# Kernel tuning notes

Hardware: AMD Instinct MI355X
Metric: run time of the kernel (lower is better)

The kernel has to match this reference:

```python
import jax, jax.numpy as jnp
import numpy as np

B = 65536
HIDDEN = 1024
NUM_LABELS = 30
MAX_OUT = 19
LABEL_IDS = [
    [0, 1, 2, 3, 5, 7, 19, 20, 28],
    [0, 1, 2, 3, 5, 7, 19, 20, 28],
    [0, 5, 7, 18, 19, 20, 22],
    [0, 1, 2, 3, 5, 7, 19, 20],
    [0, 1, 2, 3, 5, 7, 19, 20, 28],
    [0, 1, 2, 3, 5, 7, 9, 20],
    [0, 2, 4, 6, 8, 10, 12, 13, 14, 15, 16, 17, 21, 24, 26, 27],
    [0, 4, 6, 8, 10, 11, 12, 13, 14, 15, 17, 23, 24, 26, 27, 29],
    [0, 4, 6, 10, 11, 14, 15, 17, 21, 24, 25, 26, 27],
    [0, 4, 6, 7, 8, 10, 11, 12, 13, 14, 15, 17, 21, 23, 24, 26, 27, 28, 29],
    [0, 4, 6, 8, 10, 11, 12, 13, 14, 15, 16, 17, 21, 27, 29],
    [0, 4, 6, 10, 12, 15, 21, 24, 25],
]
# static remap: for head i, label l -> candidates.index(l) if present else 0
_REMAP = np.zeros((12, NUM_LABELS), dtype=np.int32)
for _i, _cand in enumerate(LABEL_IDS):
    for _j, _c in enumerate(_cand):
        _REMAP[_i, _c] = _j
REMAP = jnp.asarray(_REMAP)


def setup_inputs() -> dict:
    key = jax.random.key(0)
    k1, k2, k3, k4, k5 = jax.random.split(key, 5)
    features = jax.random.normal(k1, (B, HIDDEN), dtype=jnp.float32)
    Ws = jax.random.normal(k2, (12, HIDDEN, MAX_OUT), dtype=jnp.float32) * 0.02
    bs = jax.random.normal(k3, (12, MAX_OUT), dtype=jnp.float32) * 0.02
    head_ids = jax.random.randint(k4, (B,), 0, 12, dtype=jnp.int32)
    labels = jax.random.randint(k5, (B,), 0, NUM_LABELS, dtype=jnp.int32)
    return {"features": features, "Ws": Ws, "bs": bs,
            "head_ids": head_ids, "labels": labels}


def reference(features, Ws, bs, head_ids, labels):
    bsz = features.shape[0]
    h = jnp.tanh(features)  # FCLayer: dropout(p=0) -> tanh -> linear
    scattered = []
    total_loss = jnp.float32(0.0)
    for i, cand in enumerate(LABEL_IDS):
        n = len(cand)
        logit = h @ Ws[i][:, :n] + bs[i][:n]  # [B, n] small GEMM
        # scatter head logits into full 30-label space (base fill 1e-7)
        idx = jnp.asarray(cand, dtype=jnp.int32)
        z = jnp.full((bsz, NUM_LABELS), 1e-7, dtype=logit.dtype).at[:, idx].set(logit)
        scattered.append(z)
        # weighted CE over remapped labels (weight 0.05 for class 0, 1 otherwise)
        y = REMAP[i][labels]  # [B]
        logp = jax.nn.log_softmax(logit, axis=-1)
        nll = -jnp.take_along_axis(logp, y[:, None], axis=1)[:, 0]
        w = jnp.where(y == 0, jnp.float32(0.05), jnp.float32(1.0))
        total_loss = total_loss + jnp.sum(w * nll) / jnp.sum(w)
    cat_logits = jnp.stack(scattered, axis=1)  # [B, 12, 30]
    logits = cat_logits[jnp.arange(bsz), head_ids]  # gather by head id -> [B, 30]
    return total_loss, logits
```

## Files before the change

### kernel.cpp

```cpp
#include <hip/hip_runtime.h>
#include <cstdint>

typedef __attribute__((ext_vector_type(8)))  __bf16 bf16x8;
typedef __attribute__((ext_vector_type(16))) float  f32x16;

namespace {

constexpr int NHEADS = 12;
constexpr int TOT    = 138;
constexpr int NLBL   = 30;
constexpr int HID    = 1024;
constexpr int MAXO   = 19;
constexpr int NPAD   = 160;
constexpr int KB     = 16;
constexpr int NT     = HID / KB;
constexpr int TILE_ELE = NPAD * KB;
constexpr int EPS    = 161;

constexpr int HOFF[NHEADS + 1] = {0, 9, 18, 25, 33, 42, 50, 66, 82, 95, 114, 129, 138};
constexpr int NI[NHEADS] = {9, 9, 7, 8, 9, 8, 16, 16, 13, 19, 15, 9};
constexpr int CAND[TOT] = {
    0, 1, 2, 3, 5, 7, 19, 20, 28,
    0, 1, 2, 3, 5, 7, 19, 20, 28,
    0, 5, 7, 18, 19, 20, 22,
    0, 1, 2, 3, 5, 7, 19, 20,
    0, 1, 2, 3, 5, 7, 19, 20, 28,
    0, 1, 2, 3, 5, 7, 9, 20,
    0, 2, 4, 6, 8, 10, 12, 13, 14, 15, 16, 17, 21, 24, 26, 27,
    0, 4, 6, 8, 10, 11, 12, 13, 14, 15, 17, 23, 24, 26, 27, 29,
    0, 4, 6, 10, 11, 14, 15, 17, 21, 24, 25, 26, 27,
    0, 4, 6, 7, 8, 10, 11, 12, 13, 14, 15, 17, 21, 23, 24, 26, 27, 28, 29,
    0, 4, 6, 8, 10, 11, 12, 13, 14, 15, 16, 17, 21, 27, 29,
    0, 4, 6, 10, 12, 15, 21, 24, 25};

__device__ __forceinline__ float fast_tanh(float x) {
    float e = __expf(2.0f * x);
    return 1.0f - 2.0f * __builtin_amdgcn_rcpf(e + 1.0f);
}

__device__ __forceinline__ void head_of(int c, int& i, int& base) {
    if      (c <   9) { i = 0;  base = 0;   }
    else if (c <  18) { i = 1;  base = 9;   }
    else if (c <  25) { i = 2;  base = 18;  }
    else if (c <  33) { i = 3;  base = 25;  }
    else if (c <  42) { i = 4;  base = 33;  }
    else if (c <  50) { i = 5;  base = 42;  }
    else if (c <  66) { i = 6;  base = 50;  }
    else if (c <  82) { i = 7;  base = 66;  }
    else if (c <  95) { i = 8;  base = 82;  }
    else if (c < 114) { i = 9;  base = 95;  }
    else if (c < 129) { i = 10; base = 114; }
    else              { i = 11; base = 129; }
}

}

__global__ void pack_w_split(const float* __restrict__ Ws,
                             __bf16* __restrict__ Wh, __bf16* __restrict__ Wl) {
    const int t = blockIdx.x;
    for (int e = threadIdx.x; e < TILE_ELE; e += 256) {
        const int c  = e >> 4;
        const int kk = e & 15;
        float w = 0.0f;
        if (c < TOT) {
            int i, base;
            head_of(c, i, base);
            w = Ws[((size_t)i * HID + t * KB + kk) * MAXO + (c - base)];
        }
        __bf16 hi = (__bf16)w;
        Wh[(size_t)t * TILE_ELE + e] = hi;
        Wl[(size_t)t * TILE_ELE + e] = (__bf16)(w - (float)hi);
    }
}

__global__ __launch_bounds__(128, 1)
void fused_mfma(const float* __restrict__ F,
                const __bf16* __restrict__ Wph,
                const __bf16* __restrict__ Wpl,
                const float* __restrict__ bs,
                const int* __restrict__ head_ids,
                const int* __restrict__ labels,
                float* __restrict__ out,
                double* __restrict__ partials)
{
    __shared__ __align__(16) __bf16 htH[128 * KB];
    __shared__ __align__(16) __bf16 htL[128 * KB];
    __shared__ __align__(16) float  ep[64 * EPS];
    __shared__ float zbuf[64 * NLBL];

    const int tid  = threadIdx.x;
    const int wv   = tid >> 6;
    const int lane = tid & 63;
    const int brow = blockIdx.x * 128;

    const float* __restrict__ frow = F + (size_t)(brow + tid) * HID;
    const int boff = (lane & 31) * KB + (lane >> 5) * 8;

    f32x16 acc[2][5];
#pragma unroll
    for (int mt = 0; mt < 2; ++mt)
#pragma unroll
        for (int n = 0; n < 5; ++n)
#pragma unroll
            for (int r = 0; r < 16; ++r) acc[mt][n][r] = 0.0f;

    float4 fbA[4], fbB[4];
    bf16x8 BhA[5], BlA[5], BhB[5], BlB[5];

    {
        const float4* fp = (const float4*)frow;
#pragma unroll
        for (int q = 0; q < 4; ++q) fbA[q] = fp[q];
#pragma unroll
        for (int n = 0; n < 5; ++n) {
            BhA[n] = *(const bf16x8*)(Wph + boff + n * 512);
            BlA[n] = *(const bf16x8*)(Wpl + boff + n * 512);
        }
    }

#define STEP(FC, BHC, BLC, FN, BHN, BLN, T)                                    \
    {                                                                          \
        if ((T) + 1 < NT) {                                                    \
            const float4* fp_ = (const float4*)(frow + ((T) + 1) * KB);        \
            _Pragma("unroll") for (int q = 0; q < 4; ++q) FN[q] = fp_[q];      \
            const size_t wo_ = (size_t)((T) + 1) * TILE_ELE + boff;            \
            _Pragma("unroll") for (int n = 0; n < 5; ++n) {                    \
                BHN[n] = *(const bf16x8*)(Wph + wo_ + n * 512);                \
                BLN[n] = *(const bf16x8*)(Wpl + wo_ + n * 512);                \
            }                                                                  \
        }                                                                      \
        __syncthreads();                \
        {                                                                      \
            bf16x8 vh0, vh1, vl0, vl1;                                         \
            _Pragma("unroll") for (int q = 0; q < 4; ++q) {                    \
                float vx[4] = {FC[q].x, FC[q].y, FC[q].z, FC[q].w};            \
                _Pragma("unroll") for (int e = 0; e < 4; ++e) {                \
                    const int j = q * 4 + e;                                   \
                    float hv = fast_tanh(vx[e]);                               \
                    __bf16 hh = (__bf16)hv;                                    \
                    __bf16 hl = (__bf16)(hv - (float)hh);                      \
                    if (j < 8) { vh0[j] = hh; vl0[j] = hl; }                   \
                    else       { vh1[j - 8] = hh; vl1[j - 8] = hl; }           \
                }                                                              \
            }                                                                  \
            *(bf16x8*)&htH[tid * KB]     = vh0;                                \
            *(bf16x8*)&htH[tid * KB + 8] = vh1;                                \
            *(bf16x8*)&htL[tid * KB]     = vl0;                                \
            *(bf16x8*)&htL[tid * KB + 8] = vl1;                                \
        }                                                                      \
        __syncthreads();                                     \
        _Pragma("unroll") for (int mt = 0; mt < 2; ++mt) {                     \
            const int ab_ = (wv * 64 + mt * 32 + (lane & 31)) * KB +           \
                            (lane >> 5) * 8;                                   \
            bf16x8 ah = *(const bf16x8*)&htH[ab_];                             \
            bf16x8 al = *(const bf16x8*)&htL[ab_];                             \
            _Pragma("unroll") for (int n = 0; n < 5; ++n) {                    \
                acc[mt][n] = __builtin_amdgcn_mfma_f32_32x32x16_bf16(          \
                    ah, BHC[n], acc[mt][n], 0, 0, 0);                          \
                acc[mt][n] = __builtin_amdgcn_mfma_f32_32x32x16_bf16(          \
                    al, BHC[n], acc[mt][n], 0, 0, 0);                          \
                acc[mt][n] = __builtin_amdgcn_mfma_f32_32x32x16_bf16(          \
                    ah, BLC[n], acc[mt][n], 0, 0, 0);                          \
            }                                                                  \
        }                                                                      \
    }

    for (int t = 0; t < NT; t += 2) {
        STEP(fbA, BhA, BlA, fbB, BhB, BlB, t);
        STEP(fbB, BhB, BlB, fbA, BhA, BlA, t + 1);
    }
#undef STEP

    float wnacc[NHEADS], wdacc[NHEADS];
#pragma unroll
    for (int i = 0; i < NHEADS; ++i) { wnacc[i] = 0.0f; wdacc[i] = 0.0f; }

#pragma unroll 1
    for (int pass = 0; pass < 2; ++pass) {
        __syncthreads();
        if (wv == pass) {
#pragma unroll
            for (int mt = 0; mt < 2; ++mt)
#pragma unroll
                for (int n = 0; n < 5; ++n)
#pragma unroll
                    for (int r = 0; r < 16; ++r) {
                        const int rl = mt * 32 + (r & 3) + 8 * (r >> 2) + 4 * (lane >> 5);
                        ep[rl * EPS + n * 32 + (lane & 31)] = acc[mt][n][r];
                    }
        }
        __syncthreads();

        if (tid < 64) {
            const int row = brow + pass * 64 + tid;
            float a[TOT];
#pragma unroll
            for (int c = 0; c < TOT; ++c) a[c] = ep[tid * EPS + c];

#pragma unroll
            for (int i = 0; i < NHEADS; ++i)
#pragma unroll
                for (int j = 0; j < MAXO; ++j)
                    if (j < NI[i]) a[HOFF[i] + j] += bs[i * MAXO + j];

            const int label = labels[row];
            const int head  = head_ids[row];

#pragma unroll
            for (int i = 0; i < NHEADS; ++i) {
                int y = 0;
#pragma unroll
                for (int j = 0; j < MAXO; ++j)
                    if (j < NI[i]) { if (CAND[HOFF[i] + j] == label) y = j; }

                float m = a[HOFF[i]];
#pragma unroll
                for (int j = 1; j < MAXO; ++j)
                    if (j < NI[i]) m = fmaxf(m, a[HOFF[i] + j]);
                float s = 0.0f;
#pragma unroll
                for (int j = 0; j < MAXO; ++j)
                    if (j < NI[i]) s += __expf(a[HOFF[i] + j] - m);
                float lse = m + __logf(s);

                float ly = a[HOFF[i]];
#pragma unroll
                for (int j = 1; j < MAXO; ++j)
                    if (j < NI[i]) ly = (y == j) ? a[HOFF[i] + j] : ly;

                float w = (y == 0) ? 0.05f : 1.0f;
                wnacc[i] += w * (lse - ly);
                wdacc[i] += w;
            }

            float v[NLBL];
#pragma unroll
            for (int l = 0; l < NLBL; ++l) v[l] = 1e-7f;
#pragma unroll
            for (int i = 0; i < NHEADS; ++i) {
                if (head == i) {
#pragma unroll
                    for (int j = 0; j < MAXO; ++j)
                        if (j < NI[i]) v[CAND[HOFF[i] + j]] = a[HOFF[i] + j];
                }
            }
#pragma unroll
            for (int l = 0; l < NLBL; ++l) zbuf[tid * NLBL + l] = v[l];
        }
        __syncthreads();

        float* __restrict__ dst = out + 1 + (size_t)(brow + pass * 64) * NLBL;
        for (int q = tid; q < 64 * NLBL; q += 128) dst[q] = zbuf[q];
    }

    if (tid < 64) {
#pragma unroll
        for (int i = 0; i < NHEADS; ++i) {
#pragma unroll
            for (int off = 32; off >= 1; off >>= 1) {
                wnacc[i] += __shfl_xor(wnacc[i], off);
                wdacc[i] += __shfl_xor(wdacc[i], off);
            }
        }
        if (tid == 0) {
#pragma unroll
            for (int i = 0; i < NHEADS; ++i) {
                atomicAdd(&partials[2 * i],     (double)wnacc[i]);
                atomicAdd(&partials[2 * i + 1], (double)wdacc[i]);
            }
        }
    }
}

__global__ __launch_bounds__(128, 1)
void fused_fallback(const float* __restrict__ F,
                    const float* __restrict__ W,
                    const float* __restrict__ bs,
                    const int* __restrict__ head_ids,
                    const int* __restrict__ labels,
                    float* __restrict__ out,
                    double* __restrict__ partials)
{
    constexpr int KC = 8;
    constexpr int KSPLIT = HID / 2;
    const int tid  = threadIdx.x;
    const int wv   = tid >> 6;
    const int lane = tid & 63;
    const int row  = blockIdx.x * 64 + lane;
    const float* __restrict__ frow = F + (size_t)row * HID;

    const int kbeg = wv * KSPLIT, kend = kbeg + KSPLIT;

    float acc[TOT];
#pragma unroll
    for (int c = 0; c < TOT; ++c) acc[c] = 0.0f;

    __align__(16) float cur[KC], nxt[KC];
#pragma unroll
    for (int q = 0; q < KC / 4; ++q)
        *reinterpret_cast<float4*>(&cur[4 * q]) =
            *reinterpret_cast<const float4*>(frow + kbeg + 4 * q);

    for (int k0 = kbeg; k0 < kend; k0 += KC) {
        if (k0 + KC < kend) {
#pragma unroll
            for (int q = 0; q < KC / 4; ++q)
                *reinterpret_cast<float4*>(&nxt[4 * q]) =
                    *reinterpret_cast<const float4*>(frow + k0 + KC + 4 * q);
        }
        float h[KC];
#pragma unroll
        for (int kk = 0; kk < KC; ++kk) h[kk] = fast_tanh(cur[kk]);
#pragma unroll
        for (int kk = 0; kk < KC; ++kk) {
#pragma unroll
            for (int i = 0; i < NHEADS; ++i) {
                const float* __restrict__ wr = W + ((size_t)i * HID + (k0 + kk)) * MAXO;
#pragma unroll
                for (int j = 0; j < MAXO; ++j)
                    if (j < NI[i]) acc[HOFF[i] + j] = fmaf(h[kk], wr[j], acc[HOFF[i] + j]);
            }
        }
        if (k0 + KC < kend) {
#pragma unroll
            for (int kk = 0; kk < KC; ++kk) cur[kk] = nxt[kk];
        }
    }

    constexpr int XST = TOT + 1;
    __shared__ float xch[64 * XST];
    if (wv == 1) {
#pragma unroll
        for (int c = 0; c < TOT; ++c) xch[lane * XST + c] = acc[c];
    }
    __syncthreads();
    if (wv != 0) return;
#pragma unroll
    for (int c = 0; c < TOT; ++c) acc[c] += xch[lane * XST + c];

#pragma unroll
    for (int i = 0; i < NHEADS; ++i)
#pragma unroll
        for (int j = 0; j < MAXO; ++j)
            if (j < NI[i]) acc[HOFF[i] + j] += bs[i * MAXO + j];

    const int label = labels[row];
    const int head  = head_ids[row];
    float wn[NHEADS], wd[NHEADS];
#pragma unroll
    for (int i = 0; i < NHEADS; ++i) {
        int y = 0;
#pragma unroll
        for (int j = 0; j < MAXO; ++j)
            if (j < NI[i]) { if (CAND[HOFF[i] + j] == label) y = j; }
        float m = acc[HOFF[i]];
#pragma unroll
        for (int j = 1; j < MAXO; ++j)
            if (j < NI[i]) m = fmaxf(m, acc[HOFF[i] + j]);
        float s = 0.0f;
#pragma unroll
        for (int j = 0; j < MAXO; ++j)
            if (j < NI[i]) s += __expf(acc[HOFF[i] + j] - m);
        float lse = m + __logf(s);
        float ly = acc[HOFF[i]];
#pragma unroll
        for (int j = 1; j < MAXO; ++j)
            if (j < NI[i]) ly = (y == j) ? acc[HOFF[i] + j] : ly;
        float w = (y == 0) ? 0.05f : 1.0f;
        wn[i] = w * (lse - ly);
        wd[i] = w;
    }
#pragma unroll
    for (int i = 0; i < NHEADS; ++i) {
#pragma unroll
        for (int off = 32; off >= 1; off >>= 1) {
            wn[i] += __shfl_xor(wn[i], off);
            wd[i] += __shfl_xor(wd[i], off);
        }
    }
    if (lane == 0) {
#pragma unroll
        for (int i = 0; i < NHEADS; ++i) {
            atomicAdd(&partials[2 * i],     (double)wn[i]);
            atomicAdd(&partials[2 * i + 1], (double)wd[i]);
        }
    }
    {
        float v[NLBL];
#pragma unroll
        for (int l = 0; l < NLBL; ++l) v[l] = 1e-7f;
#pragma unroll
        for (int i = 0; i < NHEADS; ++i) {
            if (head == i) {
#pragma unroll
                for (int j = 0; j < MAXO; ++j)
                    if (j < NI[i]) v[CAND[HOFF[i] + j]] = acc[HOFF[i] + j];
            }
        }
        float* __restrict__ dst = out + 1 + (size_t)row * NLBL;
#pragma unroll
        for (int l = 0; l < NLBL; ++l) dst[l] = v[l];
    }
}

__global__ void finalize(const double* __restrict__ partials, float* __restrict__ out) {
    double t = 0.0;
    for (int i = 0; i < NHEADS; ++i) t += partials[2 * i] / partials[2 * i + 1];
    out[0] = (float)t;
}

extern "C" void kernel_launch(void* const* d_in, const int* in_sizes, int n_in,
                              void* d_out, int out_size, void* d_ws, size_t ws_size,
                              hipStream_t stream) {
    const float* F        = (const float*)d_in[0];
    const float* Ws       = (const float*)d_in[1];
    const float* bs       = (const float*)d_in[2];
    const int*   head_ids = (const int*)d_in[3];
    const int*   labels   = (const int*)d_in[4];
    float* out = (float*)d_out;

    double* partials = (double*)d_ws;
    const size_t plane_bytes = (size_t)NT * TILE_ELE * sizeof(__bf16);
    __bf16* Wph = (__bf16*)((char*)d_ws + 256);
    __bf16* Wpl = (__bf16*)((char*)d_ws + 256 + plane_bytes);
    const size_t need = 256 + 2 * plane_bytes;

    hipMemsetAsync(d_ws, 0, 2 * NHEADS * sizeof(double), stream);

    const int B = in_sizes[3];

    if (ws_size >= need) {
        pack_w_split<<<NT, 256, 0, stream>>>(Ws, Wph, Wpl);
        fused_mfma<<<B / 128, 128, 0, stream>>>(F, Wph, Wpl, bs, head_ids, labels, out, partials);
    } else {
        fused_fallback<<<B / 64, 128, 0, stream>>>(F, Ws, bs, head_ids, labels, out, partials);
    }
    finalize<<<1, 1, 0, stream>>>(partials, out);
}
```

Baseline: 495.1 us.

## Load features directly into MFMA A-operands, drop LDS staging, fuse finalize

The main kernel now uses 256 threads, and each wave owns 32 rows. Each lane loads its own slice of the feature row and builds the bf16 hi/lo A-fragments in registers, so the LDS tile and its two barriers per K step are gone. Feature prefetch is deepened to two steps ahead. The memset and finalize launches are replaced by zeroing inside the pack kernel and a last-block ticket counter that computes the loss. The epilogue is restructured per head to reduce register pressure. In exchange, each lane now issues narrower global loads, and the atomic ticket adds serialization at the end.

```diff
diff --git a/kernel.cpp b/kernel.cpp
--- a/kernel.cpp
+++ b/kernel.cpp
@@ -56,8 +56,10 @@
 }
 
 __global__ void pack_w_split(const float* __restrict__ Ws,
-                             __bf16* __restrict__ Wh, __bf16* __restrict__ Wl) {
+                             __bf16* __restrict__ Wh, __bf16* __restrict__ Wl,
+                             unsigned* __restrict__ zero_region) {
     const int t = blockIdx.x;
+    if (t == 0 && threadIdx.x < 64) zero_region[threadIdx.x] = 0u;
     for (int e = threadIdx.x; e < TILE_ELE; e += 256) {
         const int c  = e >> 4;
         const int kk = e & 15;
@@ -73,7 +75,7 @@
     }
 }
 
-__global__ __launch_bounds__(128, 1)
+__global__ __launch_bounds__(256, 2)
 void fused_mfma(const float* __restrict__ F,
                 const __bf16* __restrict__ Wph,
                 const __bf16* __restrict__ Wpl,
@@ -81,95 +83,83 @@
                 const int* __restrict__ head_ids,
                 const int* __restrict__ labels,
                 float* __restrict__ out,
-                double* __restrict__ partials)
+                double* __restrict__ partials,
+                unsigned* __restrict__ ctr)
 {
-    __shared__ __align__(16) __bf16 htH[128 * KB];
-    __shared__ __align__(16) __bf16 htL[128 * KB];
-    __shared__ __align__(16) float  ep[64 * EPS];
+    __shared__ __align__(16) float ep[64 * EPS];
     __shared__ float zbuf[64 * NLBL];
 
     const int tid  = threadIdx.x;
     const int wv   = tid >> 6;
     const int lane = tid & 63;
     const int brow = blockIdx.x * 128;
-
-    const float* __restrict__ frow = F + (size_t)(brow + tid) * HID;
+    const int row0 = brow + wv * 32 + (lane & 31);
+
+    const float* __restrict__ fptr = F + (size_t)row0 * HID + (lane >> 5) * 8;
     const int boff = (lane & 31) * KB + (lane >> 5) * 8;
 
-    f32x16 acc[2][5];
-#pragma unroll
-    for (int mt = 0; mt < 2; ++mt)
-#pragma unroll
-        for (int n = 0; n < 5; ++n)
-#pragma unroll
-            for (int r = 0; r < 16; ++r) acc[mt][n][r] = 0.0f;
-
-    float4 fbA[4], fbB[4];
-    bf16x8 BhA[5], BlA[5], BhB[5], BlB[5];
-
-    {
-        const float4* fp = (const float4*)frow;
-#pragma unroll
-        for (int q = 0; q < 4; ++q) fbA[q] = fp[q];
-#pragma unroll
-        for (int n = 0; n < 5; ++n) {
-            BhA[n] = *(const bf16x8*)(Wph + boff + n * 512);
-            BlA[n] = *(const bf16x8*)(Wpl + boff + n * 512);
-        }
-    }
-
-#define STEP(FC, BHC, BLC, FN, BHN, BLN, T)                                    \
+    f32x16 acc[5];
+#pragma unroll
+    for (int n = 0; n < 5; ++n)
+#pragma unroll
+        for (int r = 0; r < 16; ++r) acc[n][r] = 0.0f;
+
+    float4 fb0[2], fb1[2], fb2[2], fb3[2];
+    bf16x8 Bh0[5], Bl0[5], Bh1[5], Bl1[5];
+
+#define LOAD_F(D, T)                                                           \
     {                                                                          \
-        if ((T) + 1 < NT) {                                                    \
-            const float4* fp_ = (const float4*)(frow + ((T) + 1) * KB);        \
-            _Pragma("unroll") for (int q = 0; q < 4; ++q) FN[q] = fp_[q];      \
-            const size_t wo_ = (size_t)((T) + 1) * TILE_ELE + boff;            \
-            _Pragma("unroll") for (int n = 0; n < 5; ++n) {                    \
-                BHN[n] = *(const bf16x8*)(Wph + wo_ + n * 512);                \
-                BLN[n] = *(const bf16x8*)(Wpl + wo_ + n * 512);                \
+        const float* p_ = fptr + (T) * KB;                                     \
+        D[0] = *(const float4*)p_;                                             \
+        D[1] = *(const float4*)(p_ + 4);                                       \
+    }
+#define LOAD_B(BH, BL, T)                                                      \
+    {                                                                          \
+        const size_t wo_ = (size_t)(T) * TILE_ELE + boff;                      \
+        _Pragma("unroll") for (int n = 0; n < 5; ++n) {                        \
+            BH[n] = *(const bf16x8*)(Wph + wo_ + n * 512);                     \
+            BL[n] = *(const bf16x8*)(Wpl + wo_ + n * 512);                     \
+        }                                                                      \
+    }
+
+    LOAD_F(fb0, 0);
+    LOAD_F(fb1, 1);
+    LOAD_B(Bh0, Bl0, 0);
+
+#define STEP(FC, FN, BHC, BLC, BHN, BLN, T)                                    \
+    {                                                                          \
+        if ((T) + 2 < NT) LOAD_F(FN, (T) + 2);                                 \
+        if ((T) + 1 < NT) LOAD_B(BHN, BLN, (T) + 1);                           \
+        bf16x8 ah, al;                                                         \
+        _Pragma("unroll") for (int q = 0; q < 2; ++q) {                        \
+            float vx[4] = {FC[q].x, FC[q].y, FC[q].z, FC[q].w};                \
+            _Pragma("unroll") for (int e = 0; e < 4; ++e) {                    \
+                float hv = fast_tanh(vx[e]);                                   \
+                __bf16 hh = (__bf16)hv;                                        \
+                ah[q * 4 + e] = hh;                                            \
+                al[q * 4 + e] = (__bf16)(hv - (float)hh);                      \
             }                                                                  \
         }                                                                      \
-        __syncthreads();                \
-        {                                                                      \
-            bf16x8 vh0, vh1, vl0, vl1;                                         \
-            _Pragma("unroll") for (int q = 0; q < 4; ++q) {                    \
-                float vx[4] = {FC[q].x, FC[q].y, FC[q].z, FC[q].w};            \
-                _Pragma("unroll") for (int e = 0; e < 4; ++e) {                \
-                    const int j = q * 4 + e;                                   \
-                    float hv = fast_tanh(vx[e]);                               \
-                    __bf16 hh = (__bf16)hv;                                    \
-                    __bf16 hl = (__bf16)(hv - (float)hh);                      \
-                    if (j < 8) { vh0[j] = hh; vl0[j] = hl; }                   \
-                    else       { vh1[j - 8] = hh; vl1[j - 8] = hl; }           \
-                }                                                              \
-            }                                                                  \
-            *(bf16x8*)&htH[tid * KB]     = vh0;                                \
-            *(bf16x8*)&htH[tid * KB + 8] = vh1;                                \
-            *(bf16x8*)&htL[tid * KB]     = vl0;                                \
-            *(bf16x8*)&htL[tid * KB + 8] = vl1;                                \
+        _Pragma("unroll") for (int n = 0; n < 5; ++n) {                        \
+            acc[n] = __builtin_amdgcn_mfma_f32_32x32x16_bf16(                  \
+                ah, BHC[n], acc[n], 0, 0, 0);                                  \
+            acc[n] = __builtin_amdgcn_mfma_f32_32x32x16_bf16(                  \
+                al, BHC[n], acc[n], 0, 0, 0);                                  \
+            acc[n] = __builtin_amdgcn_mfma_f32_32x32x16_bf16(                  \
+                ah, BLC[n], acc[n], 0, 0, 0);                                  \
         }                                                                      \
-        __syncthreads();                                     \
-        _Pragma("unroll") for (int mt = 0; mt < 2; ++mt) {                     \
-            const int ab_ = (wv * 64 + mt * 32 + (lane & 31)) * KB +           \
-                            (lane >> 5) * 8;                                   \
-            bf16x8 ah = *(const bf16x8*)&htH[ab_];                             \
-            bf16x8 al = *(const bf16x8*)&htL[ab_];                             \
-            _Pragma("unroll") for (int n = 0; n < 5; ++n) {                    \
-                acc[mt][n] = __builtin_amdgcn_mfma_f32_32x32x16_bf16(          \
-                    ah, BHC[n], acc[mt][n], 0, 0, 0);                          \
-                acc[mt][n] = __builtin_amdgcn_mfma_f32_32x32x16_bf16(          \
-                    al, BHC[n], acc[mt][n], 0, 0, 0);                          \
-                acc[mt][n] = __builtin_amdgcn_mfma_f32_32x32x16_bf16(          \
-                    ah, BLC[n], acc[mt][n], 0, 0, 0);                          \
-            }                                                                  \
-        }                                                                      \
-    }
-
-    for (int t = 0; t < NT; t += 2) {
-        STEP(fbA, BhA, BlA, fbB, BhB, BlB, t);
-        STEP(fbB, BhB, BlB, fbA, BhA, BlA, t + 1);
+    }
+
+#pragma unroll 1
+    for (int t = 0; t < NT; t += 4) {
+        STEP(fb0, fb2, Bh0, Bl0, Bh1, Bl1, t);
+        STEP(fb1, fb3, Bh1, Bl1, Bh0, Bl0, t + 1);
+        STEP(fb2, fb0, Bh0, Bl0, Bh1, Bl1, t + 2);
+        STEP(fb3, fb1, Bh1, Bl1, Bh0, Bl0, t + 3);
     }
 #undef STEP
+#undef LOAD_B
+#undef LOAD_F
 
     float wnacc[NHEADS], wdacc[NHEADS];
 #pragma unroll
@@ -178,70 +168,62 @@
 #pragma unroll 1
     for (int pass = 0; pass < 2; ++pass) {
         __syncthreads();
-        if (wv == pass) {
-#pragma unroll
-            for (int mt = 0; mt < 2; ++mt)
-#pragma unroll
-                for (int n = 0; n < 5; ++n)
-#pragma unroll
-                    for (int r = 0; r < 16; ++r) {
-                        const int rl = mt * 32 + (r & 3) + 8 * (r >> 2) + 4 * (lane >> 5);
-                        ep[rl * EPS + n * 32 + (lane & 31)] = acc[mt][n][r];
-                    }
+        if ((wv >> 1) == pass) {
+            const int rb = (wv & 1) * 32;
+#pragma unroll
+            for (int n = 0; n < 5; ++n)
+#pragma unroll
+                for (int r = 0; r < 16; ++r) {
+                    const int rl = rb + (r & 3) + 8 * (r >> 2) + 4 * (lane >> 5);
+                    ep[rl * EPS + n * 32 + (lane & 31)] = acc[n][r];
+                }
         }
         __syncthreads();
 
         if (tid < 64) {
-            const int row = brow + pass * 64 + tid;
-            float a[TOT];
-#pragma unroll
-            for (int c = 0; c < TOT; ++c) a[c] = ep[tid * EPS + c];
-
-#pragma unroll
-            for (int i = 0; i < NHEADS; ++i)
-#pragma unroll
-                for (int j = 0; j < MAXO; ++j)
-                    if (j < NI[i]) a[HOFF[i] + j] += bs[i * MAXO + j];
-
+            const int row   = brow + pass * 64 + tid;
             const int label = labels[row];
             const int head  = head_ids[row];
 
+            float v[NLBL];
+#pragma unroll
+            for (int l = 0; l < NLBL; ++l) v[l] = 1e-7f;
+
 #pragma unroll
             for (int i = 0; i < NHEADS; ++i) {
+                float a[MAXO];
+#pragma unroll
+                for (int j = 0; j < MAXO; ++j)
+                    if (j < NI[i]) a[j] = ep[tid * EPS + HOFF[i] + j] + bs[i * MAXO + j];
+
                 int y = 0;
 #pragma unroll
                 for (int j = 0; j < MAXO; ++j)
                     if (j < NI[i]) { if (CAND[HOFF[i] + j] == label) y = j; }
 
-                float m = a[HOFF[i]];
+                float m = a[0];
 #pragma unroll
                 for (int j = 1; j < MAXO; ++j)
-                    if (j < NI[i]) m = fmaxf(m, a[HOFF[i] + j]);
+                    if (j < NI[i]) m = fmaxf(m, a[j]);
                 float s = 0.0f;
 #pragma unroll
                 for (int j = 0; j < MAXO; ++j)
-                    if (j < NI[i]) s += __expf(a[HOFF[i] + j] - m);
+                    if (j < NI[i]) s += __expf(a[j] - m);
                 float lse = m + __logf(s);
 
-                float ly = a[HOFF[i]];
+                float ly = a[0];
 #pragma unroll
                 for (int j = 1; j < MAXO; ++j)
-                    if (j < NI[i]) ly = (y == j) ? a[HOFF[i] + j] : ly;
+                    if (j < NI[i]) ly = (y == j) ? a[j] : ly;
 
                 float w = (y == 0) ? 0.05f : 1.0f;
                 wnacc[i] += w * (lse - ly);
                 wdacc[i] += w;
-            }
-
-            float v[NLBL];
-#pragma unroll
-            for (int l = 0; l < NLBL; ++l) v[l] = 1e-7f;
-#pragma unroll
-            for (int i = 0; i < NHEADS; ++i) {
+
                 if (head == i) {
 #pragma unroll
                     for (int j = 0; j < MAXO; ++j)
-                        if (j < NI[i]) v[CAND[HOFF[i] + j]] = a[HOFF[i] + j];
+                        if (j < NI[i]) v[CAND[HOFF[i] + j]] = a[j];
                 }
             }
 #pragma unroll
@@ -250,7 +232,7 @@
         __syncthreads();
 
         float* __restrict__ dst = out + 1 + (size_t)(brow + pass * 64) * NLBL;
-        for (int q = tid; q < 64 * NLBL; q += 128) dst[q] = zbuf[q];
+        for (int q = tid; q < 64 * NLBL; q += 256) dst[q] = zbuf[q];
     }
 
     if (tid < 64) {
@@ -267,6 +249,17 @@
             for (int i = 0; i < NHEADS; ++i) {
                 atomicAdd(&partials[2 * i],     (double)wnacc[i]);
                 atomicAdd(&partials[2 * i + 1], (double)wdacc[i]);
+            }
+            __threadfence();
+            unsigned ticket = atomicAdd(ctr, 1u);
+            if (ticket == gridDim.x - 1) {
+                double tt = 0.0;
+                for (int i = 0; i < NHEADS; ++i) {
+                    double n = atomicAdd(&partials[2 * i], 0.0);
+                    double d = atomicAdd(&partials[2 * i + 1], 0.0);
+                    tt += n / d;
+                }
+                out[0] = (float)tt;
             }
         }
     }
@@ -419,21 +412,22 @@
     const int*   labels   = (const int*)d_in[4];
     float* out = (float*)d_out;
 
-    double* partials = (double*)d_ws;
+    double*   partials = (double*)d_ws;
+    unsigned* ctr      = (unsigned*)((char*)d_ws + 192);
     const size_t plane_bytes = (size_t)NT * TILE_ELE * sizeof(__bf16);
     __bf16* Wph = (__bf16*)((char*)d_ws + 256);
     __bf16* Wpl = (__bf16*)((char*)d_ws + 256 + plane_bytes);
     const size_t need = 256 + 2 * plane_bytes;
 
-    hipMemsetAsync(d_ws, 0, 2 * NHEADS * sizeof(double), stream);
-
     const int B = in_sizes[3];
 
     if (ws_size >= need) {
-        pack_w_split<<<NT, 256, 0, stream>>>(Ws, Wph, Wpl);
-        fused_mfma<<<B / 128, 128, 0, stream>>>(F, Wph, Wpl, bs, head_ids, labels, out, partials);
+        pack_w_split<<<NT, 256, 0, stream>>>(Ws, Wph, Wpl, (unsigned*)d_ws);
+        fused_mfma<<<B / 128, 256, 0, stream>>>(F, Wph, Wpl, bs, head_ids, labels,
+                                                out, partials, ctr);
     } else {
+        hipMemsetAsync(d_ws, 0, 2 * NHEADS * sizeof(double), stream);
         fused_fallback<<<B / 64, 128, 0, stream>>>(F, Ws, bs, head_ids, labels, out, partials);
-    }
-    finalize<<<1, 1, 0, stream>>>(partials, out);
-}
+        finalize<<<1, 1, 0, stream>>>(partials, out);
+    }
+}
```

Result: slower. 520.1 us (+5.0%).
